# Kernel optimization log

Hardware: AMD Instinct MI355X
Metric: run time of the kernel (lower is better)

The kernel has to match this reference:

```python
import jax, jax.numpy as jnp
import numpy as np

N_NODES = 50000
N_EDGES = 800000
HID = 128

def _silu(x):
    return x * jax.nn.sigmoid(x)

def setup_inputs() -> dict:
    key = jax.random.key(0)
    ks = jax.random.split(key, 8)
    s = lambda fan_in: 1.0 / np.sqrt(fan_in)
    return {
        "h": jax.random.normal(ks[0], (N_NODES, HID), jnp.float32),
        "edges": jax.random.randint(ks[1], (2, N_EDGES), 0, N_NODES, jnp.int64),
        "distances": jax.random.uniform(ks[2], (N_EDGES, 1), jnp.float32),
        "W_e1": jax.random.normal(ks[3], (2 * HID + 1, HID), jnp.float32) * s(2 * HID + 1),
        "b_e1": jnp.zeros((HID,), jnp.float32),
        "W_e2": jax.random.normal(ks[4], (HID, HID), jnp.float32) * s(HID),
        "b_e2": jnp.zeros((HID,), jnp.float32),
        "W_ei": jax.random.normal(ks[5], (HID, 1), jnp.float32) * s(HID),
        "b_ei": jnp.zeros((1,), jnp.float32),
        "W_n1": jax.random.normal(ks[6], (HID + 1, HID), jnp.float32) * s(HID + 1),
        "b_n1": jnp.zeros((HID,), jnp.float32),
        "W_n2": jax.random.normal(ks[7], (HID, HID), jnp.float32) * s(HID),
        "b_n2": jnp.zeros((HID,), jnp.float32),
    }

def reference(h, edges, distances, W_e1, b_e1, W_e2, b_e2, W_ei, b_ei, W_n1, b_n1, W_n2, b_n2):
    row, col = edges[0], edges[1]
    # edge MLP + sigmoid gate (computed as in original; output unused downstream)
    einp = jnp.concatenate([h[row], h[col], distances], axis=1)   # [E, 2H+1]
    m = _silu(einp @ W_e1 + b_e1)
    m = _silu(m @ W_e2 + b_e2)
    edge_feat = jax.nn.sigmoid(m @ W_ei + b_ei) * m               # [E, H]
    del edge_feat  # original forward never consumes it
    # scatter-add of distances into per-node aggregate, scaled by 1/100
    agg = jax.ops.segment_sum(distances, row, num_segments=h.shape[0]) / 100.0  # [N, 1]
    # node update MLP with residual
    ninp = jnp.concatenate([h, agg], axis=-1)                      # [N, H+1]
    u = _silu(ninp @ W_n1 + b_n1) @ W_n2 + b_n2
    return h + u
```

## Files before the change

kernel.cpp:

```cpp
#include <hip/hip_runtime.h>

#define HID 128
#define NODE_PAD 50048
#define NRANGE 4
#define RANGE 12512
#define NPART 64
#define NGRP 8
#define NRED (NGRP * ((NODE_PAD / 8 + 255) / 256))

typedef __attribute__((ext_vector_type(8))) short short8;
typedef __attribute__((ext_vector_type(4))) float floatx4;

__device__ __forceinline__ short f2bf(float f) {
    unsigned u = __builtin_bit_cast(unsigned, f);
    unsigned r = (u + 0x7FFFu + ((u >> 16) & 1u)) >> 16;
    return (short)r;
}
__device__ __forceinline__ float bf2f(short s) {
    unsigned u = ((unsigned)(unsigned short)s) << 16;
    return __builtin_bit_cast(float, u);
}

__global__ __launch_bounds__(1024) void scatter_lds(const int* __restrict__ rows,
                                                    const float* __restrict__ dist,
                                                    unsigned short* __restrict__ part,
                                                    int n_edges) {
    __shared__ float bins[RANGE];
    const int i = blockIdx.x;
    const int b = (i & 7) * (NPART / 8) + (i >> 5);
    const int r = (i >> 3) & (NRANGE - 1);
    const int base = r * RANGE;

    for (int t = threadIdx.x; t < RANGE / 4; t += 1024)
        ((float4*)bins)[t] = make_float4(0.f, 0.f, 0.f, 0.f);
    __syncthreads();

    const int chunk = (n_edges + NPART - 1) / NPART;
    const int cbeg = b * chunk;
    const int cend = min(cbeg + chunk, n_edges);

    for (int e = cbeg + threadIdx.x * 4; e < cend; e += 1024 * 4) {
        if (e + 4 <= cend) {
            int4   rr = *(const int4*)(rows + e);
            float4 dd = *(const float4*)(dist + e);
            if ((unsigned)(rr.x - base) < RANGE) atomicAdd(&bins[rr.x - base], dd.x);
            if ((unsigned)(rr.y - base) < RANGE) atomicAdd(&bins[rr.y - base], dd.y);
            if ((unsigned)(rr.z - base) < RANGE) atomicAdd(&bins[rr.z - base], dd.z);
            if ((unsigned)(rr.w - base) < RANGE) atomicAdd(&bins[rr.w - base], dd.w);
        } else {
            for (int j = e; j < cend; ++j) {
                int rw = rows[j];
                if ((unsigned)(rw - base) < RANGE) atomicAdd(&bins[rw - base], dist[j]);
            }
        }
    }
    __syncthreads();

    unsigned short* dst = part + (size_t)b * NODE_PAD + base;
    for (int t = threadIdx.x; t < RANGE / 8; t += 1024) {
        float4 lo = ((const float4*)bins)[t * 2];
        float4 hi = ((const float4*)bins)[t * 2 + 1];
        short8 v;
        v[0] = f2bf(lo.x); v[1] = f2bf(lo.y); v[2] = f2bf(lo.z); v[3] = f2bf(lo.w);
        v[4] = f2bf(hi.x); v[5] = f2bf(hi.y); v[6] = f2bf(hi.z); v[7] = f2bf(hi.w);
        *(short8*)(dst + t * 8) = v;
    }
}

__global__ __launch_bounds__(256) void reduce_partials(
    const unsigned short* __restrict__ part,
    float* __restrict__ agg4,
    const float* __restrict__ W1,
    const float* __restrict__ W2,
    unsigned short* __restrict__ WT1,
    unsigned short* __restrict__ WT2) {
    if (blockIdx.x >= NRED) {
        const float* W = (blockIdx.x == NRED) ? W1 : W2;
        unsigned short* WT = (blockIdx.x == NRED) ? WT1 : WT2;
        const int col = threadIdx.x & 127;
        const int kh  = (threadIdx.x >> 7) * 64;
#pragma unroll
        for (int k8 = 0; k8 < 8; ++k8) {
            short8 v;
#pragma unroll
            for (int j = 0; j < 8; ++j)
                v[j] = f2bf(W[(size_t)(kh + k8 * 8 + j) * HID + col]);
            *(short8*)(WT + (size_t)col * HID + kh + k8 * 8) = v;
        }
        return;
    }
    const int g   = blockIdx.x & (NGRP - 1);
    const int idx = (blockIdx.x >> 3) * 256 + threadIdx.x;
    const int n8  = NODE_PAD / 8;
    if (idx < n8) {
        float s[8] = {0.f, 0.f, 0.f, 0.f, 0.f, 0.f, 0.f, 0.f};
#pragma unroll
        for (int c = 0; c < NPART / NGRP; ++c) {
            const unsigned short* p =
                part + (size_t)(g * (NPART / NGRP) + c) * NODE_PAD + idx * 8;
            short8 v = *(const short8*)p;
#pragma unroll
            for (int j = 0; j < 8; ++j) s[j] += bf2f(v[j]);
        }
        float* o = agg4 + (size_t)g * NODE_PAD + idx * 8;
        *(float4*)o       = make_float4(s[0], s[1], s[2], s[3]);
        *(float4*)(o + 4) = make_float4(s[4], s[5], s[6], s[7]);
    }
}

__global__ __launch_bounds__(512, 4) void node_mlp_mfma(
    const float* __restrict__ h,
    const float* __restrict__ agg4,
    const unsigned short* __restrict__ WT1,
    const unsigned short* __restrict__ WT2,
    const float* __restrict__ W1,
    const float* __restrict__ b1,
    const float* __restrict__ b2,
    float* __restrict__ out,
    int n_nodes)
{
    __shared__ short WL[128 * 136];
    __shared__ short t_lds[8][16 * 136];

    const int tid  = threadIdx.x;
    const int wv   = tid >> 6;
    const int lane = tid & 63;
    const int m16  = lane & 15;
    const int quad = lane >> 4;
    const int node0 = blockIdx.x * 128 + wv * 16;

    short8 w2r[4];
#pragma unroll
    for (int i = 0; i < 4; ++i)
        w2r[i] = ((const short8*)WT2)[tid + i * 512];

    short8 a1[4];
    float hkeep[4][8];
    const bool rvalid = (node0 + m16) < n_nodes;
    {
        int row = node0 + m16;
        if (row >= n_nodes) row = n_nodes - 1;
        const float* hr = h + (size_t)row * HID + quad * 8;
#pragma unroll
        for (int kc = 0; kc < 4; ++kc) {
            float4 x0 = *(const float4*)(hr + kc * 32);
            float4 x1 = *(const float4*)(hr + kc * 32 + 4);
            hkeep[kc][0] = x0.x; hkeep[kc][1] = x0.y;
            hkeep[kc][2] = x0.z; hkeep[kc][3] = x0.w;
            hkeep[kc][4] = x1.x; hkeep[kc][5] = x1.y;
            hkeep[kc][6] = x1.z; hkeep[kc][7] = x1.w;
            short8 v;
            v[0] = f2bf(x0.x); v[1] = f2bf(x0.y); v[2] = f2bf(x0.z); v[3] = f2bf(x0.w);
            v[4] = f2bf(x1.x); v[5] = f2bf(x1.y); v[6] = f2bf(x1.z); v[7] = f2bf(x1.w);
            a1[kc] = v;
        }
    }

#pragma unroll
    for (int t = tid; t < 128 * 16; t += 512) {
        short8 v = ((const short8*)WT1)[t];
        *(short8*)(WL + (t >> 4) * 136 + (t & 15) * 8) = v;
    }

    float4 a4;
    {
        float4 s = make_float4(0.f, 0.f, 0.f, 0.f);
#pragma unroll
        for (int g = 0; g < NGRP; ++g) {
            float4 p = *(const float4*)(agg4 + (size_t)g * NODE_PAD + node0 + quad * 4);
            s.x += p.x; s.y += p.y; s.z += p.z; s.w += p.w;
        }
        a4.x = s.x * 0.01f; a4.y = s.y * 0.01f; a4.z = s.z * 0.01f; a4.w = s.w * 0.01f;
    }
    __syncthreads();

#pragma unroll
    for (int nt = 0; nt < 8; ++nt) {
        floatx4 acc = {0.f, 0.f, 0.f, 0.f};
        const short* wb = WL + (nt * 16 + m16) * 136 + quad * 8;
#pragma unroll
        for (int kc = 0; kc < 4; ++kc) {
            short8 bfr = *(const short8*)(wb + kc * 32);
            acc = __builtin_amdgcn_mfma_f32_16x16x32_bf16(a1[kc], bfr, acc, 0, 0, 0);
        }
        int col = nt * 16 + m16;
        float bias = b1[col];
        float wagg = W1[(size_t)HID * HID + col];
        float av[4] = {a4.x, a4.y, a4.z, a4.w};
#pragma unroll
        for (int r = 0; r < 4; ++r) {
            float v = acc[r] + bias + av[r] * wagg;
            float sg = __builtin_amdgcn_rcpf(1.0f + __expf(-v));
            v *= sg;
            t_lds[wv][(quad * 4 + r) * 136 + col] = f2bf(v);
        }
    }

    __syncthreads();

    short8 a2[4];
#pragma unroll
    for (int kc = 0; kc < 4; ++kc)
        a2[kc] = *(const short8*)(&t_lds[wv][m16 * 136 + kc * 32 + quad * 8]);

#pragma unroll
    for (int i = 0; i < 4; ++i) {
        int t = tid + i * 512;
        *(short8*)(WL + (t >> 4) * 136 + (t & 15) * 8) = w2r[i];
    }
    __syncthreads();

    float* scratch = (float*)&t_lds[wv][0];
    const int ql = quad & 1;
    const int qh = quad >> 1;
#pragma unroll
    for (int nt = 0; nt < 8; ++nt) {
        floatx4 acc = {0.f, 0.f, 0.f, 0.f};
        const short* wb = WL + (nt * 16 + m16) * 136 + quad * 8;
#pragma unroll
        for (int kc = 0; kc < 4; ++kc) {
            short8 bfr = *(const short8*)(wb + kc * 32);
            acc = __builtin_amdgcn_mfma_f32_16x16x32_bf16(a2[kc], bfr, acc, 0, 0, 0);
        }
        float b2c = b2[nt * 16 + m16];
#pragma unroll
        for (int r = 0; r < 4; ++r)
            scratch[(quad * 4 + r) * 17 + m16] = acc[r] + b2c;
        if (qh == (nt & 1) && rvalid) {
            const int kc = nt >> 1;
            float4 s0 = *(const float4*)(scratch + m16 * 17 + ql * 8);
            float4 s1 = *(const float4*)(scratch + m16 * 17 + ql * 8 + 4);
            size_t off = (size_t)(node0 + m16) * HID + nt * 16 + ql * 8;
            float4 o0 = make_float4(hkeep[kc][0] + s0.x, hkeep[kc][1] + s0.y,
                                    hkeep[kc][2] + s0.z, hkeep[kc][3] + s0.w);
            float4 o1 = make_float4(hkeep[kc][4] + s1.x, hkeep[kc][5] + s1.y,
                                    hkeep[kc][6] + s1.z, hkeep[kc][7] + s1.w);
            *(float4*)(out + off)     = o0;
            *(float4*)(out + off + 4) = o1;
        }
    }
}

extern "C" void kernel_launch(void* const* d_in, const int* in_sizes, int n_in,
                              void* d_out, int out_size, void* d_ws, size_t ws_size,
                              hipStream_t stream) {
    const float* h     = (const float*)d_in[0];
    const int*   edges = (const int*)d_in[1];
    const float* dist  = (const float*)d_in[2];
    const float* W1    = (const float*)d_in[9];
    const float* b1    = (const float*)d_in[10];
    const float* W2    = (const float*)d_in[11];
    const float* b2    = (const float*)d_in[12];
    float* out = (float*)d_out;

    const int n_nodes = in_sizes[0] / HID;
    const int n_edges = in_sizes[2];
    const int* rows = edges;

    unsigned short* part = (unsigned short*)d_ws;
    float* agg4 = (float*)(part + (size_t)NPART * NODE_PAD);
    unsigned short* WT1 = (unsigned short*)(agg4 + (size_t)NGRP * NODE_PAD);
    unsigned short* WT2 = WT1 + HID * HID;

    scatter_lds<<<NRANGE * NPART, 1024, 0, stream>>>(rows, dist, part, n_edges);

    reduce_partials<<<NRED + 2, 256, 0, stream>>>(part, agg4, W1, W2, WT1, WT2);

    const int blocks = (n_nodes + 127) / 128;
    node_mlp_mfma<<<blocks, 512, 0, stream>>>(h, agg4, WT1, WT2, W1, b1, b2, out, n_nodes);
}
```

Measured before the change: 124.4 us.

## Finish partial reduction in-block via LDS and move weight conversion into scatter kernel

The reduce kernel now sums all 64 bf16 partials per node inside one block, using 8 slices and an LDS cross-slice reduction, and writes a single fp32 aggregate. Previously it wrote 8 partial aggregates that the node MLP re-read and summed. The bf16 weight transpose moves into two extra blocks of the scatter kernel, spread across 1024 threads, so it overlaps with the scatter. This cuts agg traffic and per-block work in the node MLP, at the cost of fewer reduce blocks and an LDS sync.

```diff
diff --git a/kernel.cpp b/kernel.cpp
--- a/kernel.cpp
+++ b/kernel.cpp
@@ -5,8 +5,10 @@
 #define NRANGE 4
 #define RANGE 12512
 #define NPART 64
-#define NGRP 8
-#define NRED (NGRP * ((NODE_PAD / 8 + 255) / 256))
+#define NGB 32
+#define NSL 8
+#define N8  (NODE_PAD / 8)
+#define NRED ((N8 + NGB - 1) / NGB)
 
 typedef __attribute__((ext_vector_type(8))) short short8;
 typedef __attribute__((ext_vector_type(4))) float floatx4;
@@ -24,9 +26,28 @@
 __global__ __launch_bounds__(1024) void scatter_lds(const int* __restrict__ rows,
                                                     const float* __restrict__ dist,
                                                     unsigned short* __restrict__ part,
+                                                    const float* __restrict__ W1,
+                                                    const float* __restrict__ W2,
+                                                    unsigned short* __restrict__ WT1,
+                                                    unsigned short* __restrict__ WT2,
                                                     int n_edges) {
     __shared__ float bins[RANGE];
     const int i = blockIdx.x;
+    if (i >= NRANGE * NPART) {
+        const float* W = (i == NRANGE * NPART) ? W1 : W2;
+        unsigned short* WT = (i == NRANGE * NPART) ? WT1 : WT2;
+        const int col = threadIdx.x & 127;
+        const int ke  = (threadIdx.x >> 7) * 16;
+#pragma unroll
+        for (int k8 = 0; k8 < 2; ++k8) {
+            short8 v;
+#pragma unroll
+            for (int j = 0; j < 8; ++j)
+                v[j] = f2bf(W[(size_t)(ke + k8 * 8 + j) * HID + col]);
+            *(short8*)(WT + (size_t)col * HID + ke + k8 * 8) = v;
+        }
+        return;
+    }
     const int b = (i & 7) * (NPART / 8) + (i >> 5);
     const int r = (i >> 3) & (NRANGE - 1);
     const int base = r * RANGE;
@@ -69,48 +90,39 @@
 
 __global__ __launch_bounds__(256) void reduce_partials(
     const unsigned short* __restrict__ part,
-    float* __restrict__ agg4,
-    const float* __restrict__ W1,
-    const float* __restrict__ W2,
-    unsigned short* __restrict__ WT1,
-    unsigned short* __restrict__ WT2) {
-    if (blockIdx.x >= NRED) {
-        const float* W = (blockIdx.x == NRED) ? W1 : W2;
-        unsigned short* WT = (blockIdx.x == NRED) ? WT1 : WT2;
-        const int col = threadIdx.x & 127;
-        const int kh  = (threadIdx.x >> 7) * 64;
-#pragma unroll
-        for (int k8 = 0; k8 < 8; ++k8) {
-            short8 v;
-#pragma unroll
-            for (int j = 0; j < 8; ++j)
-                v[j] = f2bf(W[(size_t)(kh + k8 * 8 + j) * HID + col]);
-            *(short8*)(WT + (size_t)col * HID + kh + k8 * 8) = v;
-        }
-        return;
-    }
-    const int g   = blockIdx.x & (NGRP - 1);
-    const int idx = (blockIdx.x >> 3) * 256 + threadIdx.x;
-    const int n8  = NODE_PAD / 8;
-    if (idx < n8) {
-        float s[8] = {0.f, 0.f, 0.f, 0.f, 0.f, 0.f, 0.f, 0.f};
-#pragma unroll
-        for (int c = 0; c < NPART / NGRP; ++c) {
+    float* __restrict__ agg) {
+    __shared__ float acc_lds[NSL * NGB * 8];
+
+    const int sl = threadIdx.x >> 5;
+    const int ngl = threadIdx.x & 31;
+    const int ng = blockIdx.x * NGB + ngl;
+
+    float s[8] = {0.f, 0.f, 0.f, 0.f, 0.f, 0.f, 0.f, 0.f};
+    if (ng < N8) {
+#pragma unroll
+        for (int c = 0; c < NPART / NSL; ++c) {
             const unsigned short* p =
-                part + (size_t)(g * (NPART / NGRP) + c) * NODE_PAD + idx * 8;
+                part + (size_t)(sl * (NPART / NSL) + c) * NODE_PAD + ng * 8;
             short8 v = *(const short8*)p;
 #pragma unroll
             for (int j = 0; j < 8; ++j) s[j] += bf2f(v[j]);
         }
-        float* o = agg4 + (size_t)g * NODE_PAD + idx * 8;
-        *(float4*)o       = make_float4(s[0], s[1], s[2], s[3]);
-        *(float4*)(o + 4) = make_float4(s[4], s[5], s[6], s[7]);
-    }
+    }
+#pragma unroll
+    for (int j = 0; j < 8; ++j) acc_lds[sl * (NGB * 8) + ngl * 8 + j] = s[j];
+    __syncthreads();
+
+    const int t = threadIdx.x;
+    float v = 0.f;
+#pragma unroll
+    for (int slc = 0; slc < NSL; ++slc) v += acc_lds[slc * (NGB * 8) + t];
+    const int node = blockIdx.x * (NGB * 8) + t;
+    if (node < NODE_PAD) agg[node] = v;
 }
 
 __global__ __launch_bounds__(512, 4) void node_mlp_mfma(
     const float* __restrict__ h,
-    const float* __restrict__ agg4,
+    const float* __restrict__ agg,
     const unsigned short* __restrict__ WT1,
     const unsigned short* __restrict__ WT2,
     const float* __restrict__ W1,
@@ -164,13 +176,9 @@
 
     float4 a4;
     {
-        float4 s = make_float4(0.f, 0.f, 0.f, 0.f);
-#pragma unroll
-        for (int g = 0; g < NGRP; ++g) {
-            float4 p = *(const float4*)(agg4 + (size_t)g * NODE_PAD + node0 + quad * 4);
-            s.x += p.x; s.y += p.y; s.z += p.z; s.w += p.w;
-        }
-        a4.x = s.x * 0.01f; a4.y = s.y * 0.01f; a4.z = s.z * 0.01f; a4.w = s.w * 0.01f;
+        float4 p = *(const float4*)(agg + node0 + quad * 4);
+        a4.x = p.x * 0.01f; a4.y = p.y * 0.01f;
+        a4.z = p.z * 0.01f; a4.w = p.w * 0.01f;
     }
     __syncthreads();
 
@@ -258,14 +266,15 @@
     const int* rows = edges;
 
     unsigned short* part = (unsigned short*)d_ws;
-    float* agg4 = (float*)(part + (size_t)NPART * NODE_PAD);
-    unsigned short* WT1 = (unsigned short*)(agg4 + (size_t)NGRP * NODE_PAD);
+    float* agg = (float*)(part + (size_t)NPART * NODE_PAD);
+    unsigned short* WT1 = (unsigned short*)(agg + NODE_PAD);
     unsigned short* WT2 = WT1 + HID * HID;
 
-    scatter_lds<<<NRANGE * NPART, 1024, 0, stream>>>(rows, dist, part, n_edges);
-
-    reduce_partials<<<NRED + 2, 256, 0, stream>>>(part, agg4, W1, W2, WT1, WT2);
+    scatter_lds<<<NRANGE * NPART + 2, 1024, 0, stream>>>(
+        rows, dist, part, W1, W2, WT1, WT2, n_edges);
+
+    reduce_partials<<<NRED, 256, 0, stream>>>(part, agg);
 
     const int blocks = (n_nodes + 127) / 128;
-    node_mlp_mfma<<<blocks, 512, 0, stream>>>(h, agg4, WT1, WT2, W1, b1, b2, out, n_nodes);
-}
+    node_mlp_mfma<<<blocks, 512, 0, stream>>>(h, agg, WT1, WT2, W1, b1, b2, out, n_nodes);
+}
```

After: 123.4 us. No clear change (-0.8%).
